# Kernel tuning notes

Hardware: AMD Instinct MI355X
Metric: run time of the kernel (lower is better)

Reference implementation:

```python
import jax, jax.numpy as jnp
import numpy as np

H = 4                      # attention heads
L_NAMES = ['self', 'cross'] * 3
K_LIST = [None, None, 128, 128, 64, 64]  # top-k per layer (None = full attention)
BN_EPS = 1e-5


def conv1d(x, W, b):
    # 1x1 Conv1d: x [B, Ci, N], W [Co, Ci], b [Co]
    return jnp.einsum('oi,bin->bon', W, x) + b[:, None]


def bn_eval(x, g, b):
    # BatchNorm1d in eval mode with running mean 0 / var 1
    inv = 1.0 / np.sqrt(1.0 + BN_EPS)
    return (g * inv)[:, None] * x + b[:, None]


def mha(x, src, Wq, bq, Wk, bk, Wv, bv, Wm, bm, k):
    B, D, N = x.shape
    dh = D // H
    q = conv1d(x, Wq, bq).reshape(B, dh, H, N)
    kk = conv1d(src, Wk, bk).reshape(B, dh, H, -1)
    v = conv1d(src, Wv, bv).reshape(B, dh, H, -1)
    scores = jnp.einsum('bdhn,bdhm->bhnm', q, kk) / np.sqrt(dh)  # [B,H,N,M]
    if k is None:
        p = jax.nn.softmax(scores, axis=-1)
        out = jnp.einsum('bhnm,bdhm->bdhn', p, v)
    else:
        vals, idx = jax.lax.top_k(scores, k)          # [B,H,N,k]
        S = jax.nn.softmax(vals, axis=-1)
        # gather value vectors at the top-k key indices: [B,dh,H,N,k]
        vg = jnp.take_along_axis(v[:, :, :, None, :], idx[:, None, :, :, :], axis=4)
        out = jnp.einsum('bhnk,bdhnk->bdhn', S, vg)
    return conv1d(out.reshape(B, D, N), Wm, bm)


def log_ot(scores, alpha, iters):
    b, m, n = scores.shape
    bins0 = jnp.broadcast_to(alpha, (b, m, 1))
    bins1 = jnp.broadcast_to(alpha, (b, 1, n))
    a = jnp.broadcast_to(alpha, (b, 1, 1))
    Z0 = jnp.concatenate([jnp.concatenate([scores, bins0], -1),
                          jnp.concatenate([bins1, a], -1)], 1)  # [b,m+1,n+1]
    norm = -np.log(float(m + n))
    log_mu = jnp.concatenate([jnp.full((m,), norm, scores.dtype),
                              jnp.array([np.log(float(n)) + norm], scores.dtype)])
    log_nu = jnp.concatenate([jnp.full((n,), norm, scores.dtype),
                              jnp.array([np.log(float(m)) + norm], scores.dtype)])
    log_mu = jnp.broadcast_to(log_mu, (b, m + 1))
    log_nu = jnp.broadcast_to(log_nu, (b, n + 1))

    def step(carry, _):
        u, v = carry
        u = log_mu - jax.nn.logsumexp(Z0 + v[:, None, :], axis=2)
        v = log_nu - jax.nn.logsumexp(Z0 + u[:, :, None], axis=1)
        return (u, v), None

    (u, v), _ = jax.lax.scan(step, (jnp.zeros_like(log_mu), jnp.zeros_like(log_nu)),
                             None, length=iters)
    return Z0 + u[:, :, None] + v[:, None, :] - norm


def _forward(desc0, desc1, Wq, bq, Wk, bk, Wv, bv, Wm, bm,
             W1, b1, g1, be1, W2, b2, Wf, bf, alpha, iters):
    d0, d1 = desc0, desc1
    for i, (name, k) in enumerate(zip(L_NAMES, K_LIST)):
        s0, s1 = (d1, d0) if name == 'cross' else (d0, d1)

        def prop(x, src):
            msg = mha(x, src, Wq[i], bq[i], Wk[i], bk[i], Wv[i], bv[i], Wm[i], bm[i], k)
            h = jnp.concatenate([x, msg], axis=1)           # [B, 2D, N]
            h = jax.nn.relu(bn_eval(conv1d(h, W1[i], b1[i]), g1[i], be1[i]))
            return conv1d(h, W2[i], b2[i])

        dlt0, dlt1 = prop(d0, s0), prop(d1, s1)
        d0, d1 = d0 + dlt0, d1 + dlt1
    m0 = conv1d(d0, Wf, bf)
    m1 = conv1d(d1, Wf, bf)
    scores = jnp.einsum('bdn,bdm->bnm', m0, m1) / np.sqrt(m0.shape[1])
    return log_ot(scores, alpha, iters)


def setup_inputs() -> dict:
    B, D, N, L = 4, 128, 1024, 6
    key = jax.random.key(0)
    ks = jax.random.split(key, 20)

    def nrm(k, shape, s):
        return jax.random.normal(k, shape, jnp.float32) * s

    sw = 1.0 / np.sqrt(D)
    return {
        'desc0': nrm(ks[0], (B, D, N), 1.0),
        'desc1': nrm(ks[1], (B, D, N), 1.0),
        'Wq': nrm(ks[2], (L, D, D), sw), 'bq': jnp.zeros((L, D), jnp.float32),
        'Wk': nrm(ks[3], (L, D, D), sw), 'bk': jnp.zeros((L, D), jnp.float32),
        'Wv': nrm(ks[4], (L, D, D), sw), 'bv': jnp.zeros((L, D), jnp.float32),
        'Wm': nrm(ks[5], (L, D, D), sw), 'bm': jnp.zeros((L, D), jnp.float32),
        'W1': nrm(ks[6], (L, 2 * D, 2 * D), 1.0 / np.sqrt(2 * D)),
        'b1': jnp.zeros((L, 2 * D), jnp.float32),
        'g1': jnp.ones((L, 2 * D), jnp.float32),
        'be1': jnp.zeros((L, 2 * D), jnp.float32),
        'W2': nrm(ks[7], (L, D, 2 * D), 1.0 / np.sqrt(2 * D)),
        'b2': jnp.zeros((L, D), jnp.float32),
        'Wf': nrm(ks[8], (D, D), sw), 'bf': jnp.zeros((D,), jnp.float32),
        'alpha': jnp.asarray(1.0, jnp.float32),
        'iters': 20,
    }


def reference(desc0, desc1, Wq, bq, Wk, bk, Wv, bv, Wm, bm,
              W1, b1, g1, be1, W2, b2, Wf, bf, alpha, iters):
    return _forward(desc0, desc1, Wq, bq, Wk, bk, Wv, bv, Wm, bm,
                    W1, b1, g1, be1, W2, b2, Wf, bf, alpha, iters)
```

## Files before the change

kernel.cpp:

```cpp
#include <hip/hip_runtime.h>
#include <hip/hip_fp16.h>
#include <stdint.h>

#define NPOS   1024
#define DMODEL 128
#define NP1    1025
#define PLP    1053700
#define PSTR   1028
#define PLPH   1057800
#define PSTRH  1032
#define NORMF  (-7.624618986159398f)
#define LOGN   (6.931471805599453f)

typedef __attribute__((ext_vector_type(8))) short s8v;
typedef __attribute__((ext_vector_type(4))) float f4v;
typedef unsigned short ushort_t;

#define MFMA(a, b, c) __builtin_amdgcn_mfma_f32_16x16x32_bf16((a), (b), (c), 0, 0, 0)

static __device__ __forceinline__ ushort_t f2bf(float f) {
    union { float f; uint32_t u; } c; c.f = f;
    uint32_t u = c.u;
    return (ushort_t)((u + 0x7fffu + ((u >> 16) & 1u)) >> 16);
}
static __device__ __forceinline__ uint32_t cvtpk(float lo, float hi) {
    uint32_t r;
    asm("v_cvt_pk_bf16_f32 %0, %1, %2" : "=v"(r) : "v"(lo), "v"(hi));
    return r;
}

#define NW0 294912
#define NW2 393216
#define NW3 196608
#define NW4 16384
#define NB5 2304
#define NPREP (NW0 + NW2 + NW3 + NW4 + NB5)
__global__ __launch_bounds__(256) void prep_weights(
    const float* __restrict__ Wq, const float* __restrict__ Wk, const float* __restrict__ Wv,
    const float* __restrict__ bq, const float* __restrict__ bk, const float* __restrict__ bv,
    const float* __restrict__ W1, const float* __restrict__ W2, const float* __restrict__ Wf,
    ushort_t* __restrict__ wqkv, ushort_t* __restrict__ w1c,
    ushort_t* __restrict__ w2, ushort_t* __restrict__ wf, float* __restrict__ bqkv)
{
    int idx = blockIdx.x * 256 + threadIdx.x;
    if (idx < NW0) {
        int l = idx / 49152, r2 = idx % 49152;
        int r = r2 / 128, i = r2 % 128;
        int sel = r >> 7, rr = r & 127;
        int o = ((rr & 31) << 2) + (rr >> 5);
        const float* src = sel == 0 ? Wq : (sel == 1 ? Wk : Wv);
        wqkv[idx] = f2bf(src[((size_t)l * 128 + o) * 128 + i]);
        return;
    }
    idx -= NW0;
    if (idx < NW2) {
        int i = idx & 255;
        if (i < 128) w1c[idx] = f2bf(W1[idx]);
        return;
    }
    idx -= NW2;
    if (idx < NW3) { w2[idx] = f2bf(W2[idx]); return; }
    idx -= NW3;
    if (idx < NW4) { wf[idx] = f2bf(Wf[idx]); return; }
    idx -= NW4;
    if (idx < NB5) {
        int l = idx / 384, r = idx % 384;
        int sel = r >> 7, rr = r & 127;
        int o = ((rr & 31) << 2) + (rr >> 5);
        const float* src = sel == 0 ? bq : (sel == 1 ? bk : bv);
        bqkv[idx] = src[l * 128 + o];
    }
}

#define NFOLD 196608
#define NFB   1536
__global__ __launch_bounds__(256) void fold_w1(
    const float* __restrict__ W1, const float* __restrict__ Wm,
    const float* __restrict__ b1, const float* __restrict__ bm,
    ushort_t* __restrict__ w1c, float* __restrict__ b1c)
{
    int idx = blockIdx.x * 256 + threadIdx.x;
    if (idx < NFOLD) {
        int l = idx / 32768, rem = idx % 32768;
        int o = rem / 128, ip = rem % 128;
        int i = ((ip & 31) << 2) + (ip >> 5);
        const float* w1row = W1 + ((size_t)l * 256 + o) * 256 + 128;
        const float* wmcol = Wm + (size_t)l * 16384 + i;
        float s = 0.f;
        #pragma unroll 8
        for (int j = 0; j < 128; ++j) s = fmaf(w1row[j], wmcol[(size_t)j * 128], s);
        w1c[((size_t)l * 256 + o) * 256 + 128 + ip] = f2bf(s);
        return;
    }
    idx -= NFOLD;
    if (idx < NFB) {
        int l = idx / 256, o = idx % 256;
        const float* w1row = W1 + ((size_t)l * 256 + o) * 256 + 128;
        const float* bml = bm + l * 128;
        float s = b1[l * 256 + o];
        #pragma unroll 8
        for (int j = 0; j < 128; ++j) s = fmaf(w1row[j], bml[j], s);
        b1c[idx] = s;
    }
}

__global__ __launch_bounds__(256) void transpose_in(
    const float* __restrict__ desc0, const float* __restrict__ desc1,
    float* __restrict__ df, ushort_t* __restrict__ db)
{
    int g = blockIdx.z;
    int nb = blockIdx.x << 6, cb = blockIdx.y << 5;
    __shared__ float sm[32][65];
    const float* S = (g < 4 ? desc0 : desc1);
    int gl = g & 3;
    {
        int row = threadIdx.x >> 3, c8 = (threadIdx.x & 7) << 3;
        const float* p = S + ((size_t)gl * 128 + cb + row) * NPOS + nb + c8;
        float4 v0 = *(const float4*)p;
        float4 v1 = *(const float4*)(p + 4);
        sm[row][c8 + 0] = v0.x; sm[row][c8 + 1] = v0.y; sm[row][c8 + 2] = v0.z; sm[row][c8 + 3] = v0.w;
        sm[row][c8 + 4] = v1.x; sm[row][c8 + 5] = v1.y; sm[row][c8 + 6] = v1.z; sm[row][c8 + 7] = v1.w;
    }
    __syncthreads();
    int n = threadIdx.x >> 2, cc = (threadIdx.x & 3) << 3;
    float y[8];
    #pragma unroll
    for (int e = 0; e < 8; ++e) y[e] = sm[cc + e][n];
    size_t base = ((size_t)g * NPOS + nb + n) * DMODEL + cb + cc;
    *(float4*)(df + base) = make_float4(y[0], y[1], y[2], y[3]);
    *(float4*)(df + base + 4) = make_float4(y[4], y[5], y[6], y[7]);
    uint4 pk = make_uint4(cvtpk(y[0], y[1]), cvtpk(y[2], y[3]),
                          cvtpk(y[4], y[5]), cvtpk(y[6], y[7]));
    *(uint4*)(db + base) = pk;
}

__global__ __launch_bounds__(256) void conv_mfma(
    const ushort_t* __restrict__ X0, const ushort_t* __restrict__ X1, int c0, int Ci,
    const ushort_t* __restrict__ W, const float* __restrict__ bias,
    const float* __restrict__ bn_g, const float* __restrict__ bn_b,
    float* __restrict__ resid, ushort_t* __restrict__ outb, int Co, int mode)
{
    int g = blockIdx.z;
    int nb = blockIdx.x << 6;
    int obb = blockIdx.y << 6;
    int wave = threadIdx.x >> 6, lane = threadIdx.x & 63;
    int lrow = lane & 15, lk = (lane >> 4) << 3;
    int ob = obb + (wave << 4);
    f4v acc[4] = {};
    const ushort_t* wrow = W + (size_t)(ob + lrow) * Ci + lk;
    for (int k0 = 0; k0 < Ci; k0 += 32) {
        int k = k0 + lk;
        s8v b = *(const s8v*)(wrow + k0);
        #pragma unroll
        for (int t = 0; t < 4; ++t) {
            int n = nb + (t << 4) + lrow;
            const ushort_t* xp;
            if (k < c0) xp = X0 + ((size_t)g * NPOS + n) * c0 + k;
            else        xp = X1 + ((size_t)g * NPOS + n) * (Ci - c0) + (k - c0);
            s8v a = *(const s8v*)xp;
            acc[t] = MFMA(a, b, acc[t]);
        }
    }
    __shared__ float sm[64][68];
    #pragma unroll
    for (int t = 0; t < 4; ++t)
        #pragma unroll
        for (int r = 0; r < 4; ++r)
            sm[(t << 4) + ((lane >> 4) << 2) + r][(wave << 4) + lrow] = acc[t][r];
    __syncthreads();
    const float BN_INV = 0.9999950000374997f;
    int n = threadIdx.x >> 2, oc = (threadIdx.x & 3) << 4;
    int o0 = obb + oc;
    float y[16];
    #pragma unroll
    for (int e = 0; e < 16; ++e) y[e] = sm[n][oc + e] + bias[o0 + e];
    size_t base = ((size_t)g * NPOS + nb + n) * Co + o0;
    if (mode == 1) {
        #pragma unroll
        for (int e = 0; e < 16; ++e)
            y[e] = fmaxf(bn_g[o0 + e] * BN_INV * y[e] + bn_b[o0 + e], 0.f);
    } else if (mode == 2) {
        float* rp = resid + base;
        #pragma unroll
        for (int q = 0; q < 16; q += 4) {
            float4 r4 = *(const float4*)(rp + q);
            y[q] += r4.x; y[q + 1] += r4.y; y[q + 2] += r4.z; y[q + 3] += r4.w;
            *(float4*)(rp + q) = make_float4(y[q], y[q + 1], y[q + 2], y[q + 3]);
        }
    }
    uint4 p0 = make_uint4(cvtpk(y[0], y[1]), cvtpk(y[2], y[3]),
                          cvtpk(y[4], y[5]), cvtpk(y[6], y[7]));
    uint4 p1 = make_uint4(cvtpk(y[8], y[9]), cvtpk(y[10], y[11]),
                          cvtpk(y[12], y[13]), cvtpk(y[14], y[15]));
    *(uint4*)(outb + base) = p0;
    *(uint4*)(outb + base + 8) = p1;
}

__global__ __launch_bounds__(256) void qkv_mfma(
    const ushort_t* __restrict__ X, const ushort_t* __restrict__ W,
    const float* __restrict__ bias,
    ushort_t* __restrict__ Qb, ushort_t* __restrict__ Kb, ushort_t* __restrict__ Vb)
{
    int g = blockIdx.z;
    int nb = blockIdx.x << 6;
    int obb = blockIdx.y << 6;
    int wave = threadIdx.x >> 6, lane = threadIdx.x & 63;
    int lrow = lane & 15, lk = (lane >> 4) << 3;
    int ob = obb + (wave << 4);
    f4v acc[4] = {};
    const ushort_t* wrow = W + (size_t)(ob + lrow) * DMODEL + lk;
    for (int k0 = 0; k0 < DMODEL; k0 += 32) {
        s8v b = *(const s8v*)(wrow + k0);
        #pragma unroll
        for (int t = 0; t < 4; ++t) {
            int n = nb + (t << 4) + lrow;
            s8v a = *(const s8v*)(X + ((size_t)g * NPOS + n) * DMODEL + k0 + lk);
            acc[t] = MFMA(a, b, acc[t]);
        }
    }
    __shared__ float sm[64][68];
    #pragma unroll
    for (int t = 0; t < 4; ++t)
        #pragma unroll
        for (int r = 0; r < 4; ++r)
            sm[(t << 4) + ((lane >> 4) << 2) + r][(wave << 4) + lrow] = acc[t][r];
    __syncthreads();
    if (obb < 256) {
        int n = threadIdx.x >> 2, oc = (threadIdx.x & 3) << 4;
        int ov = obb + oc;
        ushort_t* dst = (ov < 128) ? Qb : Kb;
        int c = ov & 127;
        float y[16];
        #pragma unroll
        for (int e = 0; e < 16; ++e) y[e] = sm[n][oc + e] + bias[ov + e];
        size_t base = ((size_t)g * NPOS + nb + n) * DMODEL + c;
        uint4 p0 = make_uint4(cvtpk(y[0], y[1]), cvtpk(y[2], y[3]),
                              cvtpk(y[4], y[5]), cvtpk(y[6], y[7]));
        uint4 p1 = make_uint4(cvtpk(y[8], y[9]), cvtpk(y[10], y[11]),
                              cvtpk(y[12], y[13]), cvtpk(y[14], y[15]));
        *(uint4*)(dst + base) = p0;
        *(uint4*)(dst + base + 8) = p1;
    } else {
        int c = threadIdx.x >> 2, mc = (threadIdx.x & 3) << 4;
        float bc = bias[obb + c];
        float y[16];
        #pragma unroll
        for (int e = 0; e < 16; ++e) y[e] = sm[mc + e][c] + bc;
        size_t base = ((size_t)g * DMODEL + (obb - 256) + c) * NPOS + nb + mc;
        uint4 p0 = make_uint4(cvtpk(y[0], y[1]), cvtpk(y[2], y[3]),
                              cvtpk(y[4], y[5]), cvtpk(y[6], y[7]));
        uint4 p1 = make_uint4(cvtpk(y[8], y[9]), cvtpk(y[10], y[11]),
                              cvtpk(y[12], y[13]), cvtpk(y[14], y[15]));
        *(uint4*)(Vb + base) = p0;
        *(uint4*)(Vb + base + 8) = p1;
    }
}

__global__ __launch_bounds__(512, 8) void attn_fused(
    const ushort_t* __restrict__ Qb, const ushort_t* __restrict__ Kb,
    const ushort_t* __restrict__ Vb, ushort_t* __restrict__ ao,
    int k, int cross)
{
    __shared__ ushort_t sc[16 * 1024];
    int bid = blockIdx.x;
    int gh = ((bid & 7) << 2) + (bid >> 9);
    int g = gh >> 2, h = gh & 3;
    int g2 = cross ? (g ^ 4) : g;
    int n0 = ((bid >> 3) & 63) << 4;
    int wave = threadIdx.x >> 6, lane = threadIdx.x & 63;
    int lrow = lane & 15, lq = lane >> 4;

    {
        int kq = wave;
        s8v qa = *(const s8v*)(Qb + ((size_t)g * NPOS + n0 + lrow) * DMODEL
                               + (h << 5) + (lq << 3));
        const float scale = 0.17677669529663687f;
        int swz = (lrow & 7) << 4;
        const ushort_t* kb_base = Kb + ((size_t)g2 * NPOS + (kq << 7) + lrow) * DMODEL
                                  + (h << 5) + (lq << 3);
        #pragma unroll
        for (int mt = 0; mt < 8; ++mt) {
            s8v kb = *(const s8v*)(kb_base + (size_t)mt * 16 * DMODEL);
            f4v z = {};
            z = MFMA(kb, qa, z);
            uint32_t p0 = cvtpk(z[0] * scale, z[1] * scale);
            uint32_t p1 = cvtpk(z[2] * scale, z[3] * scale);
            int m = (kq << 7) + (mt << 4);
            int byte = ((lrow << 11) + ((m + (lq << 2)) << 1)) ^ swz;
            *(uint2*)((char*)sc + byte) = make_uint2(p0, p1);
        }
    }
    __syncthreads();

    {
        bool dosel = (k < NPOS);
        for (int rr = 0; rr < 2; ++rr) {
            int row = (wave << 1) + rr;
            int swz = (row & 7) << 4;
            int base = (row << 11) + (lane << 5);
            uint4 d0 = *(const uint4*)((const char*)sc + (base ^ swz));
            uint4 d1 = *(const uint4*)((const char*)sc + ((base + 16) ^ swz));
            float val[16];
            {
                uint32_t wd[8] = {d0.x, d0.y, d0.z, d0.w, d1.x, d1.y, d1.z, d1.w};
                #pragma unroll
                for (int q = 0; q < 8; ++q) {
                    union { unsigned ui; float f; } c0, c1;
                    c0.ui = wd[q] << 16; c1.ui = wd[q] & 0xFFFF0000u;
                    val[2 * q] = c0.f; val[2 * q + 1] = c1.f;
                }
            }
            float mx = val[0];
            #pragma unroll
            for (int t = 1; t < 16; ++t) mx = fmaxf(mx, val[t]);
            #pragma unroll
            for (int o = 32; o; o >>= 1) mx = fmaxf(mx, __shfl_xor(mx, o));

            unsigned selmask = 0xFFFFu;
            if (dosel) {
                unsigned prefix = 0;
                bool exact = false;
                for (int bit = 15; bit >= 0 && !exact; --bit) {
                    unsigned cand = prefix | (1u << bit);
                    unsigned craw = (cand & 0x8000u) ? (cand ^ 0x8000u) : (cand ^ 0xFFFFu);
                    union { unsigned ui; float f; } cf; cf.ui = craw << 16;
                    float cf_f = cf.f;
                    int c = 0;
                    #pragma unroll
                    for (int t = 0; t < 16; ++t)
                        c += __popcll(__ballot(val[t] >= cf_f));
                    if (c >= k) { prefix = cand; exact = (c == k); }
                }
                unsigned praw = (prefix & 0x8000u) ? (prefix ^ 0x8000u) : (prefix ^ 0xFFFFu);
                union { unsigned ui; float f; } pf; pf.ui = praw << 16;
                float thr = pf.f;
                if (exact) {
                    selmask = 0;
                    #pragma unroll
                    for (int t = 0; t < 16; ++t)
                        selmask |= (val[t] >= thr) ? (1u << t) : 0u;
                } else {
                    int cgt = 0;
                    #pragma unroll
                    for (int t = 0; t < 16; ++t)
                        cgt += __popcll(__ballot(val[t] > thr));
                    int need = k - cgt;
                    unsigned long long lmask = (1ull << lane) - 1ull;
                    int before = 0;
                    #pragma unroll
                    for (int t = 0; t < 16; ++t)
                        before += __popcll(__ballot(val[t] == thr) & lmask);
                    int loc = 0;
                    selmask = 0;
                    #pragma unroll
                    for (int t = 0; t < 16; ++t) {
                        bool tie = (val[t] == thr);
                        if ((val[t] > thr) || (tie && (before + loc < need)))
                            selmask |= (1u << t);
                        loc += tie ? 1 : 0;
                    }
                }
            }
            float sum = 0.f;
            #pragma unroll
            for (int t = 0; t < 16; ++t) {
                float wv = ((selmask >> t) & 1u) ? __expf(val[t] - mx) : 0.f;
                val[t] = wv;
                sum += wv;
            }
            #pragma unroll
            for (int o = 32; o; o >>= 1) sum += __shfl_xor(sum, o);
            float inv = 1.f / sum;
            uint32_t ow[8];
            #pragma unroll
            for (int q = 0; q < 8; ++q)
                ow[q] = cvtpk(val[2 * q] * inv, val[2 * q + 1] * inv);
            *(uint4*)((char*)sc + (base ^ swz)) = make_uint4(ow[0], ow[1], ow[2], ow[3]);
            *(uint4*)((char*)sc + ((base + 16) ^ swz)) = make_uint4(ow[4], ow[5], ow[6], ow[7]);
        }
    }
    __syncthreads();

    {
        int kquad = wave >> 1, dimg = wave & 1;
        int db = dimg << 4;
        const ushort_t* vbase = Vb + ((size_t)g2 * DMODEL + (h << 5) + db + lrow) * NPOS
                                + (kquad << 8) + (lq << 3);
        int pswz = (lrow & 7) << 4;
        int pbase = (lrow << 11) + (kquad << 9) + (lq << 4);
        f4v acc = {};
        #pragma unroll
        for (int ks = 0; ks < 8; ++ks) {
            s8v pa = *(const s8v*)((const char*)sc + ((pbase + (ks << 6)) ^ pswz));
            s8v vv = *(const s8v*)(vbase + (ks << 5));
            acc = MFMA(pa, vv, acc);
        }
        __syncthreads();
        if (kquad > 0)
            *(f4v*)((char*)sc + (((((kquad - 1) << 1) + dimg) * 64 + lane) << 4)) = acc;
        __syncthreads();
        if (kquad == 0) {
            #pragma unroll
            for (int qq = 0; qq < 3; ++qq)
                acc = acc + *(const f4v*)((char*)sc + ((((qq << 1) + dimg) * 64 + lane) << 4));
            #pragma unroll
            for (int r = 0; r < 4; ++r) {
                int n = n0 + (lq << 2) + r;
                ao[((size_t)g * NPOS + n) * DMODEL + (h << 5) + db + lrow] = f2bf(acc[r]);
            }
        }
    }
}

__global__ __launch_bounds__(256) void final_mfma(
    const ushort_t* __restrict__ md, float* __restrict__ Z0P,
    __half* __restrict__ Z0H, __half* __restrict__ Z0TH)
{
    int b = blockIdx.z;
    int wave = threadIdx.x >> 6, lane = threadIdx.x & 63;
    int wr = wave >> 1, wc = wave & 1;
    int n0 = (blockIdx.y << 7) + (wr << 6);
    int m0 = (blockIdx.x << 7) + (wc << 6);
    int lrow = lane & 15, lk = (lane >> 4) << 3;
    f4v acc[4][4] = {};
    for (int k0 = 0; k0 < DMODEL; k0 += 32) {
        s8v qa[4], kb[4];
        #pragma unroll
        for (int t = 0; t < 4; ++t) {
            qa[t] = *(const s8v*)(md + ((size_t)b * NPOS + n0 + (t << 4) + lrow) * DMODEL + k0 + lk);
            kb[t] = *(const s8v*)(md + ((size_t)(b + 4) * NPOS + m0 + (t << 4) + lrow) * DMODEL + k0 + lk);
        }
        #pragma unroll
        for (int tn = 0; tn < 4; ++tn)
            #pragma unroll
            for (int tm = 0; tm < 4; ++tm)
                acc[tn][tm] = MFMA(qa[tn], kb[tm], acc[tn][tm]);
    }
    const float scf = 0.08838834764831845f;
    int rbase = (lane >> 4) << 2;
    #pragma unroll
    for (int tn = 0; tn < 4; ++tn) {
        #pragma unroll
        for (int tm = 0; tm < 4; ++tm) {
            #pragma unroll
            for (int r = 0; r < 4; ++r) {
                int n = n0 + (tn << 4) + rbase + r;
                int m = m0 + (tm << 4) + lrow;
                float y = acc[tn][tm][r] * scf;
                Z0P[(size_t)b * PLP + (size_t)n * PSTR + m] = y;
                __half hy = __float2half(y);
                Z0H [(size_t)b * PLPH + (size_t)n * PSTRH + m] = hy;
                Z0TH[(size_t)b * PLPH + (size_t)m * PSTRH + n] = hy;
            }
        }
    }
}

__global__ __launch_bounds__(1024) void ot_init(
    float* __restrict__ Z0P, __half* __restrict__ Z0H, __half* __restrict__ Z0TH,
    float* __restrict__ v, const float* __restrict__ alpha)
{
    float a = *alpha;
    __half ha = __float2half(a);
    int b = blockIdx.x, t = threadIdx.x;
    Z0P [(size_t)b * PLP  + (size_t)t * PSTR  + 1024] = a;
    Z0P [(size_t)b * PLP  + (size_t)1024 * PSTR + t] = a;
    Z0H [(size_t)b * PLPH + (size_t)t * PSTRH + 1024] = ha;
    Z0H [(size_t)b * PLPH + (size_t)1024 * PSTRH + t] = ha;
    Z0TH[(size_t)b * PLPH + (size_t)t * PSTRH + 1024] = ha;
    Z0TH[(size_t)b * PLPH + (size_t)1024 * PSTRH + t] = ha;
    v[b * NP1 + t] = 0.f;
    if (t == 0) {
        Z0P [(size_t)b * PLP  + (size_t)1024 * PSTR  + 1024] = a;
        Z0H [(size_t)b * PLPH + (size_t)1024 * PSTRH + 1024] = ha;
        Z0TH[(size_t)b * PLPH + (size_t)1024 * PSTRH + 1024] = ha;
        v[b * NP1 + 1024] = 0.f;
    }
}

__global__ __launch_bounds__(256) void lse_sweep_h(
    const __half* __restrict__ Z, const float* __restrict__ vin,
    float* __restrict__ uout)
{
    int wv = threadIdx.x >> 6, lane = threadIdx.x & 63;
    int r = blockIdx.x * 4 + wv;
    int b = r / NP1, i = r - b * NP1;
    const __half* z  = Z + (size_t)b * PLPH + (size_t)i * PSTRH;
    const float* vb = vin + b * NP1;
    float x[17];
    #pragma unroll
    for (int t = 0; t < 2; ++t) {
        int j = (t << 9) + (lane << 3);
        union { uint4 u; __half h[8]; } U;
        U.u = *(const uint4*)(z + j);
        float4 v0 = *(const float4*)(vb + j);
        float4 v1 = *(const float4*)(vb + j + 4);
        x[t * 8 + 0] = __half2float(U.h[0]) + v0.x;
        x[t * 8 + 1] = __half2float(U.h[1]) + v0.y;
        x[t * 8 + 2] = __half2float(U.h[2]) + v0.z;
        x[t * 8 + 3] = __half2float(U.h[3]) + v0.w;
        x[t * 8 + 4] = __half2float(U.h[4]) + v1.x;
        x[t * 8 + 5] = __half2float(U.h[5]) + v1.y;
        x[t * 8 + 6] = __half2float(U.h[6]) + v1.z;
        x[t * 8 + 7] = __half2float(U.h[7]) + v1.w;
    }
    x[16] = (lane == 0) ? (__half2float(z[1024]) + vb[1024]) : -1e30f;
    float m = x[0];
    #pragma unroll
    for (int t = 1; t < 17; ++t) m = fmaxf(m, x[t]);
    #pragma unroll
    for (int o = 32; o; o >>= 1) m = fmaxf(m, __shfl_xor(m, o));
    float sum = 0.f;
    #pragma unroll
    for (int t = 0; t < 17; ++t) sum += __expf(x[t] - m);
    #pragma unroll
    for (int o = 32; o; o >>= 1) sum += __shfl_xor(sum, o);
    if (lane == 0)
        uout[b * NP1 + i] = NORMF + ((i == 1024) ? LOGN : 0.f) - (m + __logf(sum));
}

__global__ __launch_bounds__(256) void ot_final(
    float* __restrict__ out, const float* __restrict__ Z0P,
    const float* __restrict__ u, const float* __restrict__ v)
{
    int r = blockIdx.x;
    int b = r / NP1, i = r - b * NP1;
    float ui = u[b * NP1 + i] - NORMF;
    const float* zp = Z0P + (size_t)b * PLP + (size_t)i * PSTR;
    float* zo = out + ((size_t)b * NP1 + i) * NP1;
    const float* vb = v + b * NP1;
    for (int j = threadIdx.x; j < NP1; j += 256) zo[j] = zp[j] + ui + vb[j];
}

extern "C" void kernel_launch(void* const* d_in, const int* in_sizes, int n_in,
                              void* d_out, int out_size, void* d_ws, size_t ws_size,
                              hipStream_t stream)
{
    (void)in_sizes; (void)n_in; (void)out_size; (void)ws_size;
    const float* desc0 = (const float*)d_in[0];
    const float* desc1 = (const float*)d_in[1];
    const float* Wq = (const float*)d_in[2];  const float* bq = (const float*)d_in[3];
    const float* Wk = (const float*)d_in[4];  const float* bk = (const float*)d_in[5];
    const float* Wv = (const float*)d_in[6];  const float* bv = (const float*)d_in[7];
    const float* Wm = (const float*)d_in[8];  const float* bm = (const float*)d_in[9];
    const float* W1 = (const float*)d_in[10]; const float* b1 = (const float*)d_in[11];
    const float* g1 = (const float*)d_in[12]; const float* be1 = (const float*)d_in[13];
    const float* W2 = (const float*)d_in[14]; const float* b2 = (const float*)d_in[15];
    const float* Wf = (const float*)d_in[16]; const float* bf = (const float*)d_in[17];
    const float* alpha = (const float*)d_in[18];

    float* Zout = (float*)d_out;
    float* ws = (float*)d_ws;
    size_t o = 0;
    float* d_f32      = ws;                          o += 1048576;
    ushort_t* d_bf    = (ushort_t*)(ws + o);         o += 524288;
    ushort_t* Qb      = (ushort_t*)(ws + o);         o += 524288;
    ushort_t* Kb      = (ushort_t*)(ws + o);         o += 524288;
    ushort_t* Vb      = (ushort_t*)(ws + o);         o += 524288;
    ushort_t* aob     = (ushort_t*)(ws + o);         o += 524288;
    ushort_t* hb      = (ushort_t*)(ws + o);         o += 1048576;
    ushort_t* mdesc   = (ushort_t*)(ws + o);         o += 524288;
    ushort_t* wqkv    = (ushort_t*)(ws + o);         o += 147456;
    ushort_t* w1c     = (ushort_t*)(ws + o);         o += 196608;
    ushort_t* w2w     = (ushort_t*)(ws + o);         o += 98304;
    ushort_t* wfw     = (ushort_t*)(ws + o);         o += 8192;
    float* bqkv       = ws + o;                      o += 2304;
    float* b1c        = ws + o;                      o += 1536;
    float* ub         = ws + o;                      o += 4352;
    float* vb         = ws + o;                      o += 4352;
    float* Z0P        = ws + o;                      o += 4214800;
    __half* Z0H       = (__half*)(ws + o);           o += 2115600;
    __half* Z0TH      = (__half*)(ws + o);           o += 2115600;

    dim3 blk(256);
    prep_weights<<<dim3((NPREP + 255) / 256), blk, 0, stream>>>(
        Wq, Wk, Wv, bq, bk, bv, W1, W2, Wf, wqkv, w1c, w2w, wfw, bqkv);
    fold_w1<<<dim3((NFOLD + NFB + 255) / 256), blk, 0, stream>>>(
        W1, Wm, b1, bm, w1c, b1c);
    transpose_in<<<dim3(16, 4, 8), blk, 0, stream>>>(desc0, desc1, d_f32, d_bf);

    static const int KLIST[6] = {1024, 1024, 128, 128, 64, 64};
    for (int l = 0; l < 6; ++l) {
        int cross = l & 1;
        int k = KLIST[l];
        qkv_mfma<<<dim3(16, 6, 8), blk, 0, stream>>>(
            d_bf, wqkv + (size_t)l * 49152, bqkv + l * 384, Qb, Kb, Vb);
        attn_fused<<<dim3(2048), dim3(512), 0, stream>>>(Qb, Kb, Vb, aob, k, cross);
        conv_mfma<<<dim3(16, 4, 8), blk, 0, stream>>>(
            d_bf, aob, 128, 256, w1c + (size_t)l * 65536,
            b1c + l * 256, g1 + l * 256, be1 + l * 256, nullptr, hb, 256, 1);
        conv_mfma<<<dim3(16, 2, 8), blk, 0, stream>>>(
            hb, (const ushort_t*)nullptr, 256, 256, w2w + (size_t)l * 32768,
            b2 + l * 128, nullptr, nullptr, d_f32, d_bf, 128, 2);
    }
    conv_mfma<<<dim3(16, 2, 8), blk, 0, stream>>>(
        d_bf, (const ushort_t*)nullptr, 128, 128, wfw, bf,
        nullptr, nullptr, nullptr, mdesc, 128, 0);
    final_mfma<<<dim3(8, 8, 4), blk, 0, stream>>>(mdesc, Z0P, Z0H, Z0TH);
    ot_init<<<dim3(4), dim3(1024), 0, stream>>>(Z0P, Z0H, Z0TH, vb, alpha);
    for (int it = 0; it < 20; ++it) {
        lse_sweep_h<<<dim3(1025), blk, 0, stream>>>(Z0H,  vb, ub);
        lse_sweep_h<<<dim3(1025), blk, 0, stream>>>(Z0TH, ub, vb);
    }
    ot_final<<<dim3(4100), blk, 0, stream>>>(Zout, Z0P, ub, vb);
}
```

Baseline: 746.0 us.

## Fuse MLP convolutions into one kernel and defer softmax normalization

Replaces the two per-layer MLP convolution launches with a single kernel. It computes the first conv plus BN and ReLU for a 16-position tile, keeps the hidden activations in shared memory, then runs the second conv with the residual add. This removes the global round trip for the hidden buffer and one launch per layer, but each block now does more serial work and the grid has fewer, larger blocks. Separately, attention stores unnormalized softmax weights and applies 1/sum at output time via shared memory, moving the per-element multiply off the probability path.

```diff
diff --git a/kernel.cpp b/kernel.cpp
--- a/kernel.cpp
+++ b/kernel.cpp
@@ -135,10 +135,9 @@
 }
 
 __global__ __launch_bounds__(256) void conv_mfma(
-    const ushort_t* __restrict__ X0, const ushort_t* __restrict__ X1, int c0, int Ci,
+    const ushort_t* __restrict__ X0, int Ci,
     const ushort_t* __restrict__ W, const float* __restrict__ bias,
-    const float* __restrict__ bn_g, const float* __restrict__ bn_b,
-    float* __restrict__ resid, ushort_t* __restrict__ outb, int Co, int mode)
+    ushort_t* __restrict__ outb, int Co)
 {
     int g = blockIdx.z;
     int nb = blockIdx.x << 6;
@@ -149,15 +148,11 @@
     f4v acc[4] = {};
     const ushort_t* wrow = W + (size_t)(ob + lrow) * Ci + lk;
     for (int k0 = 0; k0 < Ci; k0 += 32) {
-        int k = k0 + lk;
         s8v b = *(const s8v*)(wrow + k0);
         #pragma unroll
         for (int t = 0; t < 4; ++t) {
             int n = nb + (t << 4) + lrow;
-            const ushort_t* xp;
-            if (k < c0) xp = X0 + ((size_t)g * NPOS + n) * c0 + k;
-            else        xp = X1 + ((size_t)g * NPOS + n) * (Ci - c0) + (k - c0);
-            s8v a = *(const s8v*)xp;
+            s8v a = *(const s8v*)(X0 + ((size_t)g * NPOS + n) * Ci + k0 + lk);
             acc[t] = MFMA(a, b, acc[t]);
         }
     }
@@ -168,32 +163,103 @@
         for (int r = 0; r < 4; ++r)
             sm[(t << 4) + ((lane >> 4) << 2) + r][(wave << 4) + lrow] = acc[t][r];
     __syncthreads();
-    const float BN_INV = 0.9999950000374997f;
     int n = threadIdx.x >> 2, oc = (threadIdx.x & 3) << 4;
     int o0 = obb + oc;
     float y[16];
     #pragma unroll
     for (int e = 0; e < 16; ++e) y[e] = sm[n][oc + e] + bias[o0 + e];
     size_t base = ((size_t)g * NPOS + nb + n) * Co + o0;
-    if (mode == 1) {
-        #pragma unroll
-        for (int e = 0; e < 16; ++e)
-            y[e] = fmaxf(bn_g[o0 + e] * BN_INV * y[e] + bn_b[o0 + e], 0.f);
-    } else if (mode == 2) {
-        float* rp = resid + base;
-        #pragma unroll
-        for (int q = 0; q < 16; q += 4) {
-            float4 r4 = *(const float4*)(rp + q);
-            y[q] += r4.x; y[q + 1] += r4.y; y[q + 2] += r4.z; y[q + 3] += r4.w;
-            *(float4*)(rp + q) = make_float4(y[q], y[q + 1], y[q + 2], y[q + 3]);
-        }
-    }
     uint4 p0 = make_uint4(cvtpk(y[0], y[1]), cvtpk(y[2], y[3]),
                           cvtpk(y[4], y[5]), cvtpk(y[6], y[7]));
     uint4 p1 = make_uint4(cvtpk(y[8], y[9]), cvtpk(y[10], y[11]),
                           cvtpk(y[12], y[13]), cvtpk(y[14], y[15]));
     *(uint4*)(outb + base) = p0;
     *(uint4*)(outb + base + 8) = p1;
+}
+
+__global__ __launch_bounds__(256) void mlp_mfma(
+    const ushort_t* __restrict__ X0, const ushort_t* __restrict__ X1,
+    const ushort_t* __restrict__ W1c, const float* __restrict__ b1c,
+    const float* __restrict__ bn_g, const float* __restrict__ bn_b,
+    const ushort_t* __restrict__ W2w, const float* __restrict__ b2,
+    float* __restrict__ resid, ushort_t* __restrict__ outb)
+{
+    int g = blockIdx.y;
+    int nb = blockIdx.x << 4;
+    __shared__ ushort_t hB[16][256];
+    __shared__ float sm[16][132];
+    int wave = threadIdx.x >> 6, lane = threadIdx.x & 63;
+    int lrow = lane & 15, lk = (lane >> 4) << 3;
+    const float BN_INV = 0.9999950000374997f;
+
+    const ushort_t* x0p = X0 + ((size_t)g * NPOS + nb + lrow) * 128 + lk;
+    const ushort_t* x1p = X1 + ((size_t)g * NPOS + nb + lrow) * 128 + lk;
+    for (int p = 0; p < 4; ++p) {
+        int o = (p << 6) + (wave << 4) + lrow;
+        f4v acc = {};
+        const ushort_t* wrow = W1c + (size_t)o * 256 + lk;
+        #pragma unroll
+        for (int k0 = 0; k0 < 256; k0 += 32) {
+            s8v b = *(const s8v*)(wrow + k0);
+            s8v a = (k0 < 128) ? *(const s8v*)(x0p + k0) : *(const s8v*)(x1p + k0 - 128);
+            acc = MFMA(a, b, acc);
+        }
+        #pragma unroll
+        for (int r = 0; r < 4; ++r)
+            sm[((lane >> 4) << 2) + r][(wave << 4) + lrow] = acc[r];
+        __syncthreads();
+        {
+            int n = threadIdx.x >> 4, oc = (threadIdx.x & 15) << 2;
+            int og = (p << 6) + oc;
+            float y[4];
+            #pragma unroll
+            for (int e = 0; e < 4; ++e) {
+                float v = sm[n][oc + e] + b1c[og + e];
+                y[e] = fmaxf(bn_g[og + e] * BN_INV * v + bn_b[og + e], 0.f);
+            }
+            *(uint2*)(&hB[n][og]) = make_uint2(cvtpk(y[0], y[1]), cvtpk(y[2], y[3]));
+        }
+        __syncthreads();
+    }
+
+    f4v acc2[2] = {};
+    #pragma unroll
+    for (int k0 = 0; k0 < 256; k0 += 32) {
+        s8v a = *(const s8v*)(&hB[lrow][k0 + lk]);
+        #pragma unroll
+        for (int ot = 0; ot < 2; ++ot) {
+            int o = (wave << 5) + (ot << 4) + lrow;
+            s8v b = *(const s8v*)(W2w + (size_t)o * 256 + k0 + lk);
+            acc2[ot] = MFMA(a, b, acc2[ot]);
+        }
+    }
+    #pragma unroll
+    for (int ot = 0; ot < 2; ++ot)
+        #pragma unroll
+        for (int r = 0; r < 4; ++r)
+            sm[((lane >> 4) << 2) + r][(wave << 5) + (ot << 4) + lrow] = acc2[ot][r];
+    __syncthreads();
+    {
+        int n = threadIdx.x >> 4, oc = (threadIdx.x & 15) << 3;
+        size_t base = ((size_t)g * NPOS + nb + n) * 128 + oc;
+        float* rp = resid + base;
+        float4 ra = *(const float4*)rp;
+        float4 rb = *(const float4*)(rp + 4);
+        float y[8];
+        y[0] = sm[n][oc + 0] + b2[oc + 0] + ra.x;
+        y[1] = sm[n][oc + 1] + b2[oc + 1] + ra.y;
+        y[2] = sm[n][oc + 2] + b2[oc + 2] + ra.z;
+        y[3] = sm[n][oc + 3] + b2[oc + 3] + ra.w;
+        y[4] = sm[n][oc + 4] + b2[oc + 4] + rb.x;
+        y[5] = sm[n][oc + 5] + b2[oc + 5] + rb.y;
+        y[6] = sm[n][oc + 6] + b2[oc + 6] + rb.z;
+        y[7] = sm[n][oc + 7] + b2[oc + 7] + rb.w;
+        *(float4*)rp = make_float4(y[0], y[1], y[2], y[3]);
+        *(float4*)(rp + 4) = make_float4(y[4], y[5], y[6], y[7]);
+        uint4 pk = make_uint4(cvtpk(y[0], y[1]), cvtpk(y[2], y[3]),
+                              cvtpk(y[4], y[5]), cvtpk(y[6], y[7]));
+        *(uint4*)(outb + base) = pk;
+    }
 }
 
 __global__ __launch_bounds__(256) void qkv_mfma(
@@ -262,6 +328,7 @@
     int k, int cross)
 {
     __shared__ ushort_t sc[16 * 1024];
+    __shared__ float sinv[16];
     int bid = blockIdx.x;
     int gh = ((bid & 7) << 2) + (bid >> 9);
     int g = gh >> 2, h = gh & 3;
@@ -370,11 +437,11 @@
             }
             #pragma unroll
             for (int o = 32; o; o >>= 1) sum += __shfl_xor(sum, o);
-            float inv = 1.f / sum;
+            if (lane == 0) sinv[row] = 1.f / sum;
             uint32_t ow[8];
             #pragma unroll
             for (int q = 0; q < 8; ++q)
-                ow[q] = cvtpk(val[2 * q] * inv, val[2 * q + 1] * inv);
+                ow[q] = cvtpk(val[2 * q], val[2 * q + 1]);
             *(uint4*)((char*)sc + (base ^ swz)) = make_uint4(ow[0], ow[1], ow[2], ow[3]);
             *(uint4*)((char*)sc + ((base + 16) ^ swz)) = make_uint4(ow[4], ow[5], ow[6], ow[7]);
         }
@@ -405,8 +472,10 @@
                 acc = acc + *(const f4v*)((char*)sc + ((((qq << 1) + dimg) * 64 + lane) << 4));
             #pragma unroll
             for (int r = 0; r < 4; ++r) {
-                int n = n0 + (lq << 2) + r;
-                ao[((size_t)g * NPOS + n) * DMODEL + (h << 5) + db + lrow] = f2bf(acc[r]);
+                int rowi = (lq << 2) + r;
+                int n = n0 + rowi;
+                ao[((size_t)g * NPOS + n) * DMODEL + (h << 5) + db + lrow]
+                    = f2bf(acc[r] * sinv[rowi]);
             }
         }
     }
@@ -558,7 +627,6 @@
     ushort_t* Kb      = (ushort_t*)(ws + o);         o += 524288;
     ushort_t* Vb      = (ushort_t*)(ws + o);         o += 524288;
     ushort_t* aob     = (ushort_t*)(ws + o);         o += 524288;
-    ushort_t* hb      = (ushort_t*)(ws + o);         o += 1048576;
     ushort_t* mdesc   = (ushort_t*)(ws + o);         o += 524288;
     ushort_t* wqkv    = (ushort_t*)(ws + o);         o += 147456;
     ushort_t* w1c     = (ushort_t*)(ws + o);         o += 196608;
@@ -586,16 +654,13 @@
         qkv_mfma<<<dim3(16, 6, 8), blk, 0, stream>>>(
             d_bf, wqkv + (size_t)l * 49152, bqkv + l * 384, Qb, Kb, Vb);
         attn_fused<<<dim3(2048), dim3(512), 0, stream>>>(Qb, Kb, Vb, aob, k, cross);
-        conv_mfma<<<dim3(16, 4, 8), blk, 0, stream>>>(
-            d_bf, aob, 128, 256, w1c + (size_t)l * 65536,
-            b1c + l * 256, g1 + l * 256, be1 + l * 256, nullptr, hb, 256, 1);
-        conv_mfma<<<dim3(16, 2, 8), blk, 0, stream>>>(
-            hb, (const ushort_t*)nullptr, 256, 256, w2w + (size_t)l * 32768,
-            b2 + l * 128, nullptr, nullptr, d_f32, d_bf, 128, 2);
+        mlp_mfma<<<dim3(64, 8), blk, 0, stream>>>(
+            d_bf, aob, w1c + (size_t)l * 65536, b1c + l * 256,
+            g1 + l * 256, be1 + l * 256,
+            w2w + (size_t)l * 32768, b2 + l * 128, d_f32, d_bf);
     }
     conv_mfma<<<dim3(16, 2, 8), blk, 0, stream>>>(
-        d_bf, (const ushort_t*)nullptr, 128, 128, wfw, bf,
-        nullptr, nullptr, nullptr, mdesc, 128, 0);
+        d_bf, 128, wfw, bf, mdesc, 128);
     final_mfma<<<dim3(8, 8, 4), blk, 0, stream>>>(mdesc, Z0P, Z0H, Z0TH);
     ot_init<<<dim3(4), dim3(1024), 0, stream>>>(Z0P, Z0H, Z0TH, vb, alpha);
     for (int it = 0; it < 20; ++it) {
```

After: 755.0 us. Within noise of the previous version (+1.2%).
